# Kernel tuning notes

Measured on AMD Instinct MI355X. Metric: run time of the kernel, lower is better.

Reference implementation:

```python
import jax, jax.numpy as jnp
import numpy as np

H, W = 128, 128
HW = H * W


def _quat2mat(q):
    q = q / jnp.linalg.norm(q)
    w, x, y, z = q[0], q[1], q[2], q[3]
    return jnp.stack([
        jnp.stack([1 - 2 * (y * y + z * z), 2 * (x * y - z * w), 2 * (x * z + y * w)]),
        jnp.stack([2 * (x * y + z * w), 1 - 2 * (x * x + z * z), 2 * (y * z - x * w)]),
        jnp.stack([2 * (x * z - y * w), 2 * (y * z + x * w), 1 - 2 * (x * x + y * y)]),
    ])


def _pixel_coords():
    ys, xs = jnp.meshgrid(jnp.arange(H), jnp.arange(W), indexing='ij')
    return jnp.stack([xs.reshape(-1), ys.reshape(-1)], axis=1).astype(jnp.float32)  # [HW,2] (x,y)


def setup_inputs() -> dict:
    key = jax.random.key(0)
    k = jax.random.split(key, 6)
    N, B = 4096, 2
    positions = jax.random.normal(k[0], (N, 3), jnp.float32)
    colors = jax.random.uniform(k[1], (N, 3), dtype=jnp.float32)
    opacities = jax.random.uniform(k[2], (N, 1), dtype=jnp.float32)
    # sigma in [5,25] px so gaussians have realistic footprint on a 128x128 image
    scales = 5.0 + 20.0 * jax.random.uniform(k[3], (N, 1), dtype=jnp.float32)
    qvec = jax.random.normal(k[4], (B, 4), jnp.float32)
    # camera ~4 units back so projected depths stay positive
    tvec = jax.random.normal(k[5], (B, 3), jnp.float32) * 0.1 + jnp.array([0.0, 0.0, 4.0], jnp.float32)
    intrinsics = jnp.array([150.0, 150.0, 64.0, 64.0], jnp.float32)  # fx, fy, cx, cy
    return {
        'positions': positions, 'colors': colors, 'opacities': opacities,
        'scales': scales, 'qvec': qvec, 'tvec': tvec, 'intrinsics': intrinsics,
        'tile_hw': 8, 'chunk_gauss': 256,
    }


def reference(positions, colors, opacities, scales, qvec, tvec, intrinsics, tile_hw, chunk_gauss):
    N = positions.shape[0]
    n_chunks = -(-N // chunk_gauss)  # eps is added once per gaussian chunk in the original
    fx, fy, cx, cy = intrinsics[0], intrinsics[1], intrinsics[2], intrinsics[3]
    coords = _pixel_coords()                      # [HW,2]
    c2 = (coords ** 2).sum(-1)                    # [HW]
    var = scales[:, 0] ** 2                       # [N]

    def render_one(q, t):
        R = _quat2mat(q)
        p = positions @ R.T + t                   # [N,3] camera-space
        proj = jnp.stack([p[:, 0] / p[:, 2] * fx + cx,
                          p[:, 1] / p[:, 2] * fy + cy], axis=1)  # [N,2]
        # ||coords - proj||^2 expanded so the cross term is a GEMM
        dist2 = (proj ** 2).sum(-1)[:, None] + c2[None, :] - 2.0 * (proj @ coords.T)  # [N,HW]
        w = opacities * jnp.exp(-0.5 * dist2 / var[:, None])   # [N,HW]
        num = jnp.einsum('np,nc->pc', w, colors)                # [HW,3]
        den = w.sum(0)[:, None] + n_chunks * 1e-8               # [HW,1]
        img = (num / jnp.maximum(den, 1e-8)).T                  # [3,HW]
        img = img.reshape(3, HW // tile_hw, tile_hw)
        return img[:, :H, :W]                                   # -> (3, H, tile_hw), as in source

    return jax.vmap(render_one)(qvec, tvec)
```

## Files before the change

kernel.cpp:

```cpp
#include <hip/hip_runtime.h>
#include <stdint.h>

#define IMG_H 128
#define IMG_W 128

__global__ __launch_bounds__(256, 1)
void gs_render(const float* __restrict__ pos,
               const float* __restrict__ col,
               const float* __restrict__ opa,
               const float* __restrict__ scl,
               const float* __restrict__ qvec,
               const float* __restrict__ tvec,
               const float* __restrict__ intr,
               const int* __restrict__ chunkg,
               float* __restrict__ out,
               int N, int P, int tiles_per_batch)
{
    __shared__ float4 ldsA[4096];

    const int tid  = threadIdx.x;
    const int b    = blockIdx.x / tiles_per_batch;
    const int tile = blockIdx.x % tiles_per_batch;

    {
        float qw = qvec[b * 4 + 0];
        float qx = qvec[b * 4 + 1];
        float qy = qvec[b * 4 + 2];
        float qz = qvec[b * 4 + 3];
        float qn = rsqrtf(qw * qw + qx * qx + qy * qy + qz * qz);
        qw *= qn; qx *= qn; qy *= qn; qz *= qn;

        const float r00 = 1.0f - 2.0f * (qy * qy + qz * qz);
        const float r01 = 2.0f * (qx * qy - qz * qw);
        const float r02 = 2.0f * (qx * qz + qy * qw);
        const float r10 = 2.0f * (qx * qy + qz * qw);
        const float r11 = 1.0f - 2.0f * (qx * qx + qz * qz);
        const float r12 = 2.0f * (qy * qz - qx * qw);
        const float r20 = 2.0f * (qx * qz - qy * qw);
        const float r21 = 2.0f * (qy * qz + qx * qw);
        const float r22 = 1.0f - 2.0f * (qx * qx + qy * qy);

        const float tx = tvec[b * 3 + 0];
        const float ty = tvec[b * 3 + 1];
        const float tz = tvec[b * 3 + 2];

        const float fx = intr[0];
        const float fy = intr[1];
        const float cx = intr[2];
        const float cy = intr[3];

        for (int g = tid; g < N && g < 4096; g += 256) {
            float p0 = pos[3 * g + 0];
            float p1 = pos[3 * g + 1];
            float p2 = pos[3 * g + 2];

            float X = r00 * p0 + r01 * p1 + r02 * p2 + tx;
            float Y = r10 * p0 + r11 * p1 + r12 * p2 + ty;
            float Z = r20 * p0 + r21 * p1 + r22 * p2 + tz;

            float invZ = __fdividef(1.0f, Z);
            float u = X * invZ * fx + cx;
            float v = Y * invZ * fy + cy;

            float s   = scl[g];
            float var = s * s;
            float k   = -0.5f * __fdividef(1.0f, var);
            float op  = opa[g];
            float L   = __logf(fmaxf(op, 1e-30f));
            float c0  = fmaf(k, u * u + v * v, L);

            ldsA[g] = make_float4(-2.0f * k * u, -2.0f * k * v, c0, k);
        }
    }
    __syncthreads();

    const int wave = tid >> 6;
    const int lane = tid & 63;

    const int p0 = tile * 8 + wave * 2;
    const int p1 = p0 + 1;
    const float x0 = (float)(p0 & (IMG_W - 1));
    const float y0 = (float)(p0 >> 7);
    const float x1 = (float)(p1 & (IMG_W - 1));
    const float y1 = (float)(p1 >> 7);
    const float c20 = x0 * x0 + y0 * y0;
    const float c21 = x1 * x1 + y1 * y1;

    float d0 = 0.f, r0 = 0.f, g0 = 0.f, b0 = 0.f;
    float d1 = 0.f, r1 = 0.f, g1 = 0.f, b1 = 0.f;

    const int iters = N >> 6;
#pragma unroll 4
    for (int i = 0; i < iters; ++i) {
        const int g = (i << 6) | lane;
        float4 A = ldsA[g];

        const float* cp = col + 3 * g;
        float cr = cp[0];
        float cg = cp[1];
        float cb = cp[2];

        float t0 = fmaf(A.x, x0, fmaf(A.y, y0, fmaf(A.w, c20, A.z)));
        float t1 = fmaf(A.x, x1, fmaf(A.y, y1, fmaf(A.w, c21, A.z)));
        float w0 = __expf(t0);
        float w1 = __expf(t1);

        d0 += w0;              d1 += w1;
        r0 = fmaf(w0, cr, r0); r1 = fmaf(w1, cr, r1);
        g0 = fmaf(w0, cg, g0); g1 = fmaf(w1, cg, g1);
        b0 = fmaf(w0, cb, b0); b1 = fmaf(w1, cb, b1);
    }

#pragma unroll
    for (int m = 32; m >= 1; m >>= 1) {
        d0 += __shfl_xor(d0, m, 64);
        r0 += __shfl_xor(r0, m, 64);
        g0 += __shfl_xor(g0, m, 64);
        b0 += __shfl_xor(b0, m, 64);
        d1 += __shfl_xor(d1, m, 64);
        r1 += __shfl_xor(r1, m, 64);
        g1 += __shfl_xor(g1, m, 64);
        b1 += __shfl_xor(b1, m, 64);
    }

    if (lane == 0) {
        int cg  = chunkg[0];
        int nch = (N + cg - 1) / cg;
        float eps = (float)nch * 1e-8f;

        float inv0 = 1.0f / fmaxf(d0 + eps, 1e-8f);
        float inv1 = 1.0f / fmaxf(d1 + eps, 1e-8f);

        float* ob = out + (size_t)b * 3 * P;
        ob[0 * P + p0] = r0 * inv0;
        ob[1 * P + p0] = g0 * inv0;
        ob[2 * P + p0] = b0 * inv0;
        ob[0 * P + p1] = r1 * inv1;
        ob[1 * P + p1] = g1 * inv1;
        ob[2 * P + p1] = b1 * inv1;
    }
}

extern "C" void kernel_launch(void* const* d_in, const int* in_sizes, int n_in,
                              void* d_out, int out_size, void* d_ws, size_t ws_size,
                              hipStream_t stream) {
    const float* pos  = (const float*)d_in[0];
    const float* col  = (const float*)d_in[1];
    const float* opa  = (const float*)d_in[2];
    const float* scl  = (const float*)d_in[3];
    const float* qv   = (const float*)d_in[4];
    const float* tv   = (const float*)d_in[5];
    const float* intr = (const float*)d_in[6];
    const int* chunkg = (const int*)d_in[8];
    float* out        = (float*)d_out;

    const int N = in_sizes[0] / 3;
    const int B = in_sizes[4] / 4;
    const int P = out_size / (3 * B);
    const int tiles = P / 8;

    gs_render<<<dim3(B * tiles), dim3(256), 0, stream>>>(
        pos, col, opa, scl, qv, tv, intr, chunkg, out, N, P, tiles);
}
```

Baseline: 81.52 us.

## Split gaussian loop across four wave slices per pixel pair with LDS reduction

Blocks grow from 256 to 1024 threads. Each pair of pixels is now handled by four waves, each covering a quarter of the gaussians, and the partial sums are combined through shared memory by eight threads. The aim is to shorten the per-block serial loop and amortize the per-block gaussian projection into LDS over more compute. The cost is an extra barrier and reduction step, plus different occupancy and register limits from the larger block size.

```diff
diff --git a/kernel.cpp b/kernel.cpp
--- a/kernel.cpp
+++ b/kernel.cpp
@@ -1,10 +1,9 @@
 #include <hip/hip_runtime.h>
 #include <stdint.h>
 
-#define IMG_H 128
 #define IMG_W 128
 
-__global__ __launch_bounds__(256, 1)
+__global__ __launch_bounds__(1024)
 void gs_render(const float* __restrict__ pos,
                const float* __restrict__ col,
                const float* __restrict__ opa,
@@ -17,6 +16,7 @@
                int N, int P, int tiles_per_batch)
 {
     __shared__ float4 ldsA[4096];
+    __shared__ float  part[16][8];
 
     const int tid  = threadIdx.x;
     const int b    = blockIdx.x / tiles_per_batch;
@@ -49,7 +49,7 @@
         const float cx = intr[2];
         const float cy = intr[3];
 
-        for (int g = tid; g < N && g < 4096; g += 256) {
+        for (int g = tid; g < N && g < 4096; g += 1024) {
             float p0 = pos[3 * g + 0];
             float p1 = pos[3 * g + 1];
             float p2 = pos[3 * g + 2];
@@ -74,10 +74,12 @@
     }
     __syncthreads();
 
-    const int wave = tid >> 6;
-    const int lane = tid & 63;
+    const int wave  = tid >> 6;
+    const int lane  = tid & 63;
+    const int pp    = wave & 3;
+    const int slice = wave >> 2;
 
-    const int p0 = tile * 8 + wave * 2;
+    const int p0 = tile * 8 + pp * 2;
     const int p1 = p0 + 1;
     const float x0 = (float)(p0 & (IMG_W - 1));
     const float y0 = (float)(p0 >> 7);
@@ -89,10 +91,13 @@
     float d0 = 0.f, r0 = 0.f, g0 = 0.f, b0 = 0.f;
     float d1 = 0.f, r1 = 0.f, g1 = 0.f, b1 = 0.f;
 
-    const int iters = N >> 6;
-#pragma unroll 4
+    const int slice_len = N >> 2;
+    const int iters     = slice_len >> 6;
+    const int base      = slice * slice_len;
+
+#pragma unroll 8
     for (int i = 0; i < iters; ++i) {
-        const int g = (i << 6) | lane;
+        const int g = base + (i << 6) + lane;
         float4 A = ldsA[g];
 
         const float* cp = col + 3 * g;
@@ -124,20 +129,38 @@
     }
 
     if (lane == 0) {
+        part[wave][0] = d0; part[wave][1] = r0;
+        part[wave][2] = g0; part[wave][3] = b0;
+        part[wave][4] = d1; part[wave][5] = r1;
+        part[wave][6] = g1; part[wave][7] = b1;
+    }
+    __syncthreads();
+
+    if (tid < 8) {
+        const int p    = tid;
+        const int ppix = p >> 1;
+        const int off  = (p & 1) * 4;
+
+        float d = 0.f, r = 0.f, g = 0.f, bl = 0.f;
+#pragma unroll
+        for (int s = 0; s < 4; ++s) {
+            const int w = (s << 2) | ppix;
+            d  += part[w][off + 0];
+            r  += part[w][off + 1];
+            g  += part[w][off + 2];
+            bl += part[w][off + 3];
+        }
+
         int cg  = chunkg[0];
         int nch = (N + cg - 1) / cg;
         float eps = (float)nch * 1e-8f;
+        float inv = 1.0f / fmaxf(d + eps, 1e-8f);
 
-        float inv0 = 1.0f / fmaxf(d0 + eps, 1e-8f);
-        float inv1 = 1.0f / fmaxf(d1 + eps, 1e-8f);
-
+        const int px = tile * 8 + p;
         float* ob = out + (size_t)b * 3 * P;
-        ob[0 * P + p0] = r0 * inv0;
-        ob[1 * P + p0] = g0 * inv0;
-        ob[2 * P + p0] = b0 * inv0;
-        ob[0 * P + p1] = r1 * inv1;
-        ob[1 * P + p1] = g1 * inv1;
-        ob[2 * P + p1] = b1 * inv1;
+        ob[0 * P + px] = r  * inv;
+        ob[1 * P + px] = g  * inv;
+        ob[2 * P + px] = bl * inv;
     }
 }
 
@@ -159,6 +182,6 @@
     const int P = out_size / (3 * B);
     const int tiles = P / 8;
 
-    gs_render<<<dim3(B * tiles), dim3(256), 0, stream>>>(
+    gs_render<<<dim3(B * tiles), dim3(1024), 0, stream>>>(
         pos, col, opa, scl, qv, tv, intr, chunkg, out, N, P, tiles);
 }
```

New measurement: 77.95 us. 4.4% less time.
